# Optimization experiments

Measured on AMD Instinct MI355X. Metric: run time of the kernel, lower is better.

The kernel has to match this reference:

```python
import jax, jax.numpy as jnp
import numpy as np
import math

N_LAYER = 3
D = 256
NH = 4
MULT = 128
N = MULT * D // NH  # 8192
VOCAB = 256
EPS = 1e-5
TWO_PI = 2.0 * math.pi


def _get_freqs(n, theta=2.0 ** 16):
    t = jnp.arange(0, n, dtype=jnp.float32)
    q = jnp.floor(t / 2.0) * 2.0  # quantize to pairs
    return 1.0 / (theta ** (q / n)) / TWO_PI  # [N]


def _ln(x):
    # LayerNorm over last dim, no affine
    mu = jnp.mean(x, axis=-1, keepdims=True)
    var = jnp.var(x, axis=-1, keepdims=True)
    return (x - mu) / jnp.sqrt(var + EPS)


def _rope(phases, v):
    # phases: [T, N] (cycles); v: [..., T, N]
    ph = (phases % 1.0) * TWO_PI
    c, s = jnp.cos(ph), jnp.sin(ph)
    v_rot = jnp.stack((-v[..., 1::2], v[..., ::2]), axis=-1).reshape(v.shape)
    return v * c + v_rot * s


def setup_inputs() -> dict:
    key = jax.random.key(0)
    ks = jax.random.split(key, 6)
    B, T = 1, 1024
    std = 0.02
    return {
        "idx": jax.random.randint(ks[0], (B, T), 0, VOCAB),
        "embed": jax.random.normal(ks[1], (VOCAB, D), jnp.float32) * std,
        "encoder": jax.random.normal(ks[2], (NH, D, N), jnp.float32) * std,
        "encoder_v": jax.random.normal(ks[3], (NH, D, N), jnp.float32) * std,
        "decoder": jax.random.normal(ks[4], (NH * N, D), jnp.float32) * std,
        "lm_head": jax.random.normal(ks[5], (D, VOCAB), jnp.float32) * std,
    }


def reference(idx, embed, encoder, encoder_v, decoder, lm_head):
    B, T = idx.shape
    freqs = _get_freqs(N)  # [N]
    phases = jnp.arange(T, dtype=jnp.float32)[:, None] * freqs[None, :]  # [T, N]
    # strict lower triangular causal mask (diagonal excluded)
    causal = jnp.tril(jnp.ones((T, T), dtype=jnp.bool_), k=-1)

    x = _ln(embed[idx])  # [B, T, D]
    for _ in range(N_LAYER):
        # encoder projection + ReLU sparsification: [B, nh, T, N]
        x_sparse = jax.nn.relu(jnp.einsum('btd,hdn->bhtn', x, encoder))
        # RoPE on Q (= K)
        qr = _rope(phases, x_sparse)
        # unnormalized bilinear causal attention (no softmax)
        scores = jnp.einsum('bhtn,bhsn->bhts', qr, qr)
        scores = jnp.where(causal, scores, 0.0)
        ykv = _ln(jnp.einsum('bhts,bsd->bhtd', scores, x))  # [B, nh, T, D]
        y_sparse = jax.nn.relu(jnp.einsum('bhtd,hdn->bhtn', ykv, encoder_v))
        xy = x_sparse * y_sparse  # [B, nh, T, N]
        # MLP decode: head-major flatten of (nh, N) matches decoder rows
        ymlp = jnp.einsum('bhtn,btd... wrong', xy) if False else (
            xy.transpose(0, 2, 1, 3).reshape(B, T, NH * N) @ decoder)  # [B, T, D]
        x = _ln(x + _ln(ymlp))
    logits = x @ lm_head  # [B, T, VOCAB]
    return logits
```

## Files before the change

kernel.cpp:

```cpp
#include <hip/hip_runtime.h>
#include <hip/hip_bf16.h>
#include <math.h>
#include <stdint.h>

#define T_SEQ 1024
#define D_DIM 256
#define NH_C 4
#define N_DIM 8192
#define VOCAB_C 256
#define NLAYER 3
#define TWO_PI_F 6.283185307179586f
#define KSPLIT_DEC 32
#define KSPLIT_SC 2

typedef __bf16 bf16x8 __attribute__((ext_vector_type(8)));
typedef float f32x4 __attribute__((ext_vector_type(4)));

__device__ __forceinline__ unsigned short f2bf(float f) {
  unsigned u = __builtin_bit_cast(unsigned, f);
  u += 0x7fffu + ((u >> 16) & 1u);
  return (unsigned short)(u >> 16);
}
__device__ __forceinline__ float bf2f(unsigned short h) {
  unsigned u = ((unsigned)h) << 16;
  return __builtin_bit_cast(float, u);
}
__device__ __forceinline__ unsigned pack2(float a, float b) {
  return (unsigned)f2bf(a) | ((unsigned)f2bf(b) << 16);
}

typedef __attribute__((address_space(3))) uint32_t lds_u32;
typedef __attribute__((address_space(1))) const uint32_t glob_u32;
__device__ __forceinline__ void gload_lds16(const void* g, void* l) {
  __builtin_amdgcn_global_load_lds(reinterpret_cast<glob_u32*>(reinterpret_cast<uintptr_t>(g)),
                                   reinterpret_cast<lds_u32*>(reinterpret_cast<uintptr_t>(l)), 16, 0,
                                   0);
}

__global__ void k_transpose(const float* __restrict__ src, unsigned short* __restrict__ dst,
                            int R, int C, long sB, long dB) {
  __shared__ float tile[32][33];
  const int b = blockIdx.z;
  src += (size_t)b * sB;
  dst += (size_t)b * dB;
  const int c0 = blockIdx.x * 32, r0 = blockIdx.y * 32;
  const int tx = threadIdx.x, ty = threadIdx.y;
#pragma unroll
  for (int i = 0; i < 32; i += 8)
    tile[ty + i][tx] = src[(size_t)(r0 + ty + i) * C + (c0 + tx)];
  __syncthreads();
#pragma unroll
  for (int i = 0; i < 32; i += 8)
    dst[(size_t)(c0 + ty + i) * R + (r0 + tx)] = f2bf(tile[tx][ty + i]);
}

__global__ void k_ropetab(unsigned* __restrict__ cs) {
  const int id = blockIdx.x * 256 + threadIdx.x;
  const int pair = id >> 10, t = id & 1023;
  const float freq = exp2f(-(float)pair * (1.0f / 256.0f)) * (1.0f / TWO_PI_F);
  float ph = (float)t * freq;
  ph -= floorf(ph);
  float s, c;
  __sincosf(ph * TWO_PI_F, &s, &c);
  cs[id] = pack2(c, s);
}

__device__ __forceinline__ void stats256(float4 v, float& mu, float& rs) {
  float s = v.x + v.y + v.z + v.w;
  float ss = v.x * v.x + v.y * v.y + v.z * v.z + v.w * v.w;
#pragma unroll
  for (int o = 1; o < 64; o <<= 1) { s += __shfl_xor(s, o); ss += __shfl_xor(ss, o); }
  mu = s * (1.0f / 256.0f);
  float var = ss * (1.0f / 256.0f) - mu * mu;
  rs = rsqrtf(var + 1e-5f);
}

__global__ void k_embed_ln(const int* __restrict__ idx, const float* __restrict__ embed,
                           float* __restrict__ x, unsigned short* __restrict__ xb,
                           unsigned short* __restrict__ xT) {
  const int t = blockIdx.x, lane = threadIdx.x;
  const float* row = embed + (size_t)idx[t] * D_DIM;
  float4 v = ((const float4*)row)[lane];
  float mu, rs;
  stats256(v, mu, rs);
  float4 o = make_float4((v.x - mu) * rs, (v.y - mu) * rs, (v.z - mu) * rs, (v.w - mu) * rs);
  ((float4*)(x + (size_t)t * D_DIM))[lane] = o;
  ((uint2*)(xb + (size_t)t * D_DIM))[lane] = make_uint2(pack2(o.x, o.y), pack2(o.z, o.w));
  const int d0 = lane * 4;
  xT[(size_t)(d0 + 0) * T_SEQ + t] = f2bf(o.x);
  xT[(size_t)(d0 + 1) * T_SEQ + t] = f2bf(o.y);
  xT[(size_t)(d0 + 2) * T_SEQ + t] = f2bf(o.z);
  xT[(size_t)(d0 + 3) * T_SEQ + t] = f2bf(o.w);
}

__global__ void k_ln_rows(const float* __restrict__ in, unsigned short* __restrict__ outb) {
  const int r = blockIdx.x, lane = threadIdx.x;
  float4 v = ((const float4*)(in + (size_t)r * D_DIM))[lane];
  float mu, rs;
  stats256(v, mu, rs);
  ((uint2*)(outb + (size_t)r * D_DIM))[lane] =
      make_uint2(pack2((v.x - mu) * rs, (v.y - mu) * rs), pack2((v.z - mu) * rs, (v.w - mu) * rs));
}

template <int NP>
__global__ void k_update_x(const float* __restrict__ ymlp, float* __restrict__ x,
                           unsigned short* __restrict__ xb, unsigned short* __restrict__ xT) {
  const int t = blockIdx.x, lane = threadIdx.x;
  float4 m = make_float4(0.f, 0.f, 0.f, 0.f);
#pragma unroll
  for (int pp = 0; pp < NP; ++pp) {
    float4 q = ((const float4*)(ymlp + (size_t)pp * T_SEQ * D_DIM + (size_t)t * D_DIM))[lane];
    m.x += q.x; m.y += q.y; m.z += q.z; m.w += q.w;
  }
  float mu1, rs1;
  stats256(m, mu1, rs1);
  float4 xv = ((const float4*)(x + (size_t)t * D_DIM))[lane];
  float4 z = make_float4(xv.x + (m.x - mu1) * rs1, xv.y + (m.y - mu1) * rs1,
                         xv.z + (m.z - mu1) * rs1, xv.w + (m.w - mu1) * rs1);
  float mu2, rs2;
  stats256(z, mu2, rs2);
  float4 o = make_float4((z.x - mu2) * rs2, (z.y - mu2) * rs2, (z.z - mu2) * rs2, (z.w - mu2) * rs2);
  ((float4*)(x + (size_t)t * D_DIM))[lane] = o;
  ((uint2*)(xb + (size_t)t * D_DIM))[lane] = make_uint2(pack2(o.x, o.y), pack2(o.z, o.w));
  const int d0 = lane * 4;
  xT[(size_t)(d0 + 0) * T_SEQ + t] = f2bf(o.x);
  xT[(size_t)(d0 + 1) * T_SEQ + t] = f2bf(o.y);
  xT[(size_t)(d0 + 2) * T_SEQ + t] = f2bf(o.z);
  xT[(size_t)(d0 + 3) * T_SEQ + t] = f2bf(o.w);
}

template <int NP>
__global__ void k_comb(const float* __restrict__ sp, unsigned short* __restrict__ sc) {
  const size_t gid = (size_t)blockIdx.x * 256 + threadIdx.x;
  const size_t e0 = gid * 8;
  const int s = (int)(e0 & (T_SEQ - 1));
  const int t = (int)((e0 >> 10) & (T_SEQ - 1));
  if (s >= t) return;
  const int h = (int)(e0 >> 20);
  float v[8] = {0.f, 0.f, 0.f, 0.f, 0.f, 0.f, 0.f, 0.f};
#pragma unroll
  for (int pp = 0; pp < NP; ++pp) {
    const float* a = sp + ((size_t)(h * NP + pp)) * T_SEQ * T_SEQ + (size_t)t * T_SEQ + s;
    float4 a0 = *(const float4*)a, a1 = *(const float4*)(a + 4);
    v[0] += a0.x; v[1] += a0.y; v[2] += a0.z; v[3] += a0.w;
    v[4] += a1.x; v[5] += a1.y; v[6] += a1.z; v[7] += a1.w;
  }
  unsigned short o[8];
#pragma unroll
  for (int j = 0; j < 8; ++j) o[j] = (s + j < t) ? f2bf(v[j]) : (unsigned short)0;
  *(uint4*)(sc + e0) = *(uint4*)o;
}

template <int MODE, int BM, int BN, bool TRI_A, bool SWAPXY>
__global__ __launch_bounds__(256) void k_gemm(const unsigned short* __restrict__ A, long lda, long sAz,
                                              const unsigned short* __restrict__ B, long ldb, long sBz,
                                              void* __restrict__ Cv, long ldc, long sCz,
                                              const unsigned short* __restrict__ extra, long sEz,
                                              unsigned short* __restrict__ C2,
                                              const unsigned* __restrict__ ctab, int Ksize) {
  constexpr int MF = BM / 32;
  constexpr int NF = BN / 32;
  constexpr int BUFB = (BM + BN) * 128;

  const unsigned nbx = gridDim.x, nby = gridDim.y;
  const unsigned total = nbx * nby * gridDim.z;
  const unsigned lid = (blockIdx.z * nby + blockIdx.y) * nbx + blockIdx.x;
  const unsigned qq = total >> 3, rr = total & 7;
  const unsigned xcd = lid & 7, loc = lid >> 3;
  const unsigned wg = (xcd < rr ? xcd * (qq + 1) : rr * (qq + 1) + (xcd - rr) * qq) + loc;

  int bx, by, bz, zAB, kbase = 0;
  if constexpr (MODE == 2 || MODE == 6) {
    constexpr int NRT = T_SEQ / BM;
    constexpr int TPH = NRT * (NRT + 1) / 2;
    const int zz = wg / TPH;
    const int tt = wg % TPH;
    by = (int)((sqrtf(8.0f * (float)tt + 1.0f) - 1.0f) * 0.5f);
    if (by > NRT - 1) by = NRT - 1;
    while ((by + 1) * (by + 2) / 2 <= tt) ++by;
    while (by * (by + 1) / 2 > tt) --by;
    bx = tt - by * (by + 1) / 2;
    bz = zz;
    if constexpr (MODE == 6) {
      zAB = zz >> 1;
      kbase = (zz & 1) * Ksize;
    } else {
      zAB = zz;
    }
  } else if constexpr (SWAPXY) {
    by = wg % nby;
    bx = (wg / nby) % nbx;
    bz = wg / (nbx * nby);
    zAB = bz;
  } else {
    bx = wg % nbx;
    by = (wg / nbx) % nby;
    bz = wg / (nbx * nby);
    zAB = bz;
  }
  if constexpr (MODE == 7) kbase = bz * Ksize;

  const int i0 = by * BM;
  const int j0 = bx * BN;

  A += (size_t)zAB * sAz;
  B += (size_t)zAB * sBz;
  float* Cf = (float*)Cv + (size_t)bz * sCz;
  unsigned short* Ch = (unsigned short*)Cv + (size_t)bz * sCz;
  unsigned short* C2h = C2 ? C2 + (size_t)bz * sCz : nullptr;
  const unsigned short* E = extra ? extra + (size_t)bz * sEz : nullptr;

  const int tid = threadIdx.x;
  const int lane = tid & 63, w = tid >> 6;
  const int wr = w >> 1, wc = w & 1;

  __shared__ __align__(16) char lds[2 * BUFB];

  f32x4 acc[MF][NF];
#pragma unroll
  for (int m = 0; m < MF; ++m)
#pragma unroll
    for (int n = 0; n < NF; ++n) acc[m][n] = f32x4{0.f, 0.f, 0.f, 0.f};

  const char* Abytes = (const char*)A;
  const char* Bbytes = (const char*)B;
  const size_t ldab = (size_t)((MODE == 7) ? N_DIM : lda) * 2;
  const size_t ldbb = (size_t)ldb * 2;
  const int lr = lane >> 3;
  const int scol = ((lane & 7) * 16) ^ (lr << 4);

  auto stage = [&](int buf, int kt) {
    const int kk = kbase + kt * 64;
    const char* Ag;
    if constexpr (MODE == 7) {
      Ag = Abytes +
           ((size_t)(kk >> 13) * ((size_t)T_SEQ * N_DIM) + (size_t)i0 * N_DIM + (kk & (N_DIM - 1))) * 2;
    } else {
      Ag = Abytes + ((size_t)i0 * lda + kk) * 2;
    }
    const char* Bg = Bbytes + ((size_t)j0 * ldb + kk) * 2;
    char* lb = lds + buf * BUFB;
#pragma unroll
    for (int it = 0; it < BM / 32; ++it) {
      const int r0 = (w + 4 * it) * 8;
      gload_lds16(Ag + (size_t)(r0 + lr) * ldab + scol, lb + r0 * 128);
    }
#pragma unroll
    for (int it = 0; it < BN / 32; ++it) {
      const int r0 = (w + 4 * it) * 8;
      gload_lds16(Bg + (size_t)(r0 + lr) * ldbb + scol, lb + BM * 128 + r0 * 128);
    }
  };

  const int ar = lane & 15;
  const int ko16 = (lane >> 4) * 16;
  const int swz = (lane & 7) << 4;

  auto compute = [&](const char* Ab) {
    const char* Bb = Ab + BM * 128;
    bf16x8 af[2][MF], bfr[2][NF];
#pragma unroll
    for (int kk = 0; kk < 2; ++kk) {
      const int koff = (kk * 64 + ko16) ^ swz;
#pragma unroll
      for (int m = 0; m < MF; ++m)
        af[kk][m] = *(const bf16x8*)(Ab + (size_t)(wr * (BM / 2) + m * 16 + ar) * 128 + koff);
#pragma unroll
      for (int n = 0; n < NF; ++n)
        bfr[kk][n] = *(const bf16x8*)(Bb + (size_t)(wc * (BN / 2) + n * 16 + ar) * 128 + koff);
    }
#pragma unroll
    for (int kk = 0; kk < 2; ++kk)
#pragma unroll
      for (int m = 0; m < MF; ++m)
#pragma unroll
        for (int n = 0; n < NF; ++n)
          acc[m][n] = __builtin_amdgcn_mfma_f32_16x16x32_bf16(af[kk][m], bfr[kk][n], acc[m][n], 0, 0, 0);
  };

  const int nt = TRI_A ? (i0 / 64 + BM / 64) : Ksize / 64;
  stage(0, 0);
  __syncthreads();
  int cur = 0;
  for (int t = 0; t < nt; ++t) {
    if (t + 1 < nt) stage(cur ^ 1, t + 1);
    compute(lds + cur * BUFB);
    __syncthreads();
    cur ^= 1;
  }

#pragma unroll
  for (int m = 0; m < MF; ++m) {
    const int row0 = i0 + wr * (BM / 2) + m * 16 + ((lane >> 4) << 2);
#pragma unroll
    for (int n = 0; n < NF; ++n) {
      const int col = j0 + wc * (BN / 2) + n * 16 + (lane & 15);
      f32x4 c = acc[m][n];
      if constexpr (MODE == 4) {
        const uint4 q = *(const uint4*)(ctab + (size_t)(col >> 1) * T_SEQ + row0);
        const unsigned qw[4] = {q.x, q.y, q.z, q.w};
        const float sgn = (lane & 1) ? 1.f : -1.f;
#pragma unroll
        for (int r = 0; r < 4; ++r) {
          const float v = fmaxf(c[r], 0.f);
          const float pv = __shfl_xor(v, 1);
          const float cc = bf2f((unsigned short)(qw[r] & 0xffffu));
          const float ss = bf2f((unsigned short)(qw[r] >> 16));
          Ch[(size_t)(row0 + r) * ldc + col] = f2bf(v);
          C2h[(size_t)(row0 + r) * ldc + col] = f2bf(v * cc + sgn * pv * ss);
        }
      } else {
#pragma unroll
        for (int r = 0; r < 4; ++r) {
          const int row = row0 + r;
          const float v = c[r];
          if constexpr (MODE == 0 || MODE == 6 || MODE == 7) {
            Cf[(size_t)row * ldc + col] = v;
          } else if constexpr (MODE == 2) {
            Ch[(size_t)row * ldc + col] = (col < row) ? f2bf(v) : (unsigned short)0;
          } else if constexpr (MODE == 3) {
            float g = bf2f(E[(size_t)row * ldc + col]);
            Ch[(size_t)row * ldc + col] = f2bf(fmaxf(v, 0.f) * g);
          }
        }
      }
    }
  }
}

extern "C" void kernel_launch(void* const* d_in, const int* in_sizes, int n_in,
                              void* d_out, int out_size, void* d_ws, size_t ws_size,
                              hipStream_t stream) {
  const int* idx = (const int*)d_in[0];
  const float* embed = (const float*)d_in[1];
  const float* enc = (const float*)d_in[2];
  const float* encv = (const float*)d_in[3];
  const float* dec = (const float*)d_in[4];
  const float* lmh = (const float*)d_in[5];
  float* out = (float*)d_out;

  char* p = (char*)d_ws;
  auto carve = [&](size_t bytes) -> void* {
    void* r = (void*)p;
    p += (bytes + 255) & ~(size_t)255;
    return r;
  };
  unsigned short* encT = (unsigned short*)carve((size_t)NH_C * N_DIM * D_DIM * 2);
  unsigned short* encvT = (unsigned short*)carve((size_t)NH_C * N_DIM * D_DIM * 2);
  unsigned short* decT = (unsigned short*)carve((size_t)D_DIM * NH_C * N_DIM * 2);
  unsigned short* lmT = (unsigned short*)carve((size_t)VOCAB_C * D_DIM * 2);
  float* x = (float*)carve((size_t)T_SEQ * D_DIM * 4);
  unsigned short* xb = (unsigned short*)carve((size_t)T_SEQ * D_DIM * 2);
  unsigned short* xT = (unsigned short*)carve((size_t)D_DIM * T_SEQ * 2);
  unsigned short* xs = (unsigned short*)carve((size_t)NH_C * T_SEQ * N_DIM * 2);
  unsigned short* qr = (unsigned short*)carve((size_t)NH_C * T_SEQ * N_DIM * 2);
  unsigned short* sc = (unsigned short*)carve((size_t)NH_C * T_SEQ * T_SEQ * 2);
  float* ykv = (float*)carve((size_t)NH_C * T_SEQ * D_DIM * 4);
  unsigned short* ykvln = (unsigned short*)carve((size_t)NH_C * T_SEQ * D_DIM * 2);
  float* ymlp = (float*)carve((size_t)KSPLIT_DEC * T_SEQ * D_DIM * 4);
  unsigned* cstab = (unsigned*)carve((size_t)(N_DIM / 2) * T_SEQ * 4);
  float* scf32 = (float*)carve((size_t)KSPLIT_SC * NH_C * T_SEQ * T_SEQ * 4);
  const bool split_ok = ((size_t)(p - (char*)d_ws) <= ws_size);

  const dim3 tb32(32, 8);
  k_transpose<<<dim3(N_DIM / 32, D_DIM / 32, NH_C), tb32, 0, stream>>>(
      enc, encT, D_DIM, N_DIM, (long)D_DIM * N_DIM, (long)N_DIM * D_DIM);
  k_transpose<<<dim3(N_DIM / 32, D_DIM / 32, NH_C), tb32, 0, stream>>>(
      encv, encvT, D_DIM, N_DIM, (long)D_DIM * N_DIM, (long)N_DIM * D_DIM);
  k_transpose<<<dim3(D_DIM / 32, (NH_C * N_DIM) / 32, 1), tb32, 0, stream>>>(
      dec, decT, NH_C * N_DIM, D_DIM, 0, 0);
  k_transpose<<<dim3(VOCAB_C / 32, D_DIM / 32, 1), tb32, 0, stream>>>(lmh, lmT, D_DIM, VOCAB_C, 0, 0);
  k_ropetab<<<((N_DIM / 2) * T_SEQ) / 256, 256, 0, stream>>>(cstab);
  k_embed_ln<<<T_SEQ, 64, 0, stream>>>(idx, embed, x, xb, xT);
  (void)hipMemsetAsync(sc, 0, (size_t)NH_C * T_SEQ * T_SEQ * 2, stream);

  for (int l = 0; l < NLAYER; ++l) {
    k_gemm<4, 128, 128, false, true><<<dim3(N_DIM / 128, T_SEQ / 128, NH_C), 256, 0, stream>>>(
        xb, D_DIM, 0, encT, D_DIM, (long)N_DIM * D_DIM, xs, N_DIM, (long)T_SEQ * N_DIM, nullptr, 0,
        qr, cstab, D_DIM);
    if (split_ok) {
      k_gemm<6, 128, 128, false, false>
          <<<dim3(KSPLIT_SC * NH_C * (T_SEQ / 128) * (T_SEQ / 128 + 1) / 2, 1, 1), 256, 0, stream>>>(
              qr, N_DIM, (long)T_SEQ * N_DIM, qr, N_DIM, (long)T_SEQ * N_DIM, scf32, T_SEQ,
              (long)T_SEQ * T_SEQ, nullptr, 0, nullptr, nullptr, N_DIM / KSPLIT_SC);
      k_comb<KSPLIT_SC><<<(NH_C * T_SEQ * T_SEQ / 8) / 256, 256, 0, stream>>>(scf32, sc);
    } else {
      k_gemm<2, 64, 64, false, false>
          <<<dim3(NH_C * (T_SEQ / 64) * (T_SEQ / 64 + 1) / 2, 1, 1), 256, 0, stream>>>(
              qr, N_DIM, (long)T_SEQ * N_DIM, qr, N_DIM, (long)T_SEQ * N_DIM, sc, T_SEQ,
              (long)T_SEQ * T_SEQ, nullptr, 0, nullptr, nullptr, N_DIM);
    }
    k_gemm<0, 64, 64, true, false><<<dim3(D_DIM / 64, T_SEQ / 64, NH_C), 256, 0, stream>>>(
        sc, T_SEQ, (long)T_SEQ * T_SEQ, xT, T_SEQ, 0, ykv, D_DIM, (long)T_SEQ * D_DIM, nullptr, 0,
        nullptr, nullptr, T_SEQ);
    k_ln_rows<<<NH_C * T_SEQ, 64, 0, stream>>>(ykv, ykvln);
    k_gemm<3, 128, 128, false, true><<<dim3(N_DIM / 128, T_SEQ / 128, NH_C), 256, 0, stream>>>(
        ykvln, D_DIM, (long)T_SEQ * D_DIM, encvT, D_DIM, (long)N_DIM * D_DIM, qr, N_DIM,
        (long)T_SEQ * N_DIM, xs, (long)T_SEQ * N_DIM, nullptr, nullptr, D_DIM);
    k_gemm<7, 128, 128, false, false>
        <<<dim3(D_DIM / 128, T_SEQ / 128, KSPLIT_DEC), 256, 0, stream>>>(
            qr, N_DIM, 0, decT, (long)(NH_C * N_DIM), 0, ymlp, D_DIM, (long)T_SEQ * D_DIM,
            nullptr, 0, nullptr, nullptr, (NH_C * N_DIM) / KSPLIT_DEC);
    k_update_x<KSPLIT_DEC><<<T_SEQ, 64, 0, stream>>>(ymlp, x, xb, xT);
  }
  k_gemm<0, 64, 64, false, false><<<dim3(VOCAB_C / 64, T_SEQ / 64, 1), 256, 0, stream>>>(
      xb, D_DIM, 0, lmT, D_DIM, 0, out, VOCAB_C, 0, nullptr, 0, nullptr, nullptr, D_DIM);
}
```

Before: 667.1 us.

## Drop x_sparse buffer by inverting RoPE from qr in gate epilogue

The encoder GEMM now writes only the rotated qr tensor, stored as packed pairs, instead of both x_sparse and qr. The encoder_v GEMM recovers x_sparse by applying the inverse rotation to qr in place and uses it as the gate. This removes one large bf16 write and read per layer and frees workspace, which lets the score split-K be raised from 2 to 4. The trade-off is extra bf16 rounding on the recovered gate and in-place aliasing of qr.

```diff
diff --git a/kernel.cpp b/kernel.cpp
--- a/kernel.cpp
+++ b/kernel.cpp
@@ -11,7 +11,7 @@
 #define NLAYER 3
 #define TWO_PI_F 6.283185307179586f
 #define KSPLIT_DEC 32
-#define KSPLIT_SC 2
+#define KSPLIT_SC 4
 
 typedef __bf16 bf16x8 __attribute__((ext_vector_type(8)));
 typedef float f32x4 __attribute__((ext_vector_type(4)));
@@ -154,8 +154,8 @@
 template <int MODE, int BM, int BN, bool TRI_A, bool SWAPXY>
 __global__ __launch_bounds__(256) void k_gemm(const unsigned short* __restrict__ A, long lda, long sAz,
                                               const unsigned short* __restrict__ B, long ldb, long sBz,
-                                              void* __restrict__ Cv, long ldc, long sCz,
-                                              const unsigned short* __restrict__ extra, long sEz,
+                                              void* Cv, long ldc, long sCz,
+                                              const unsigned short* extra, long sEz,
                                               unsigned short* __restrict__ C2,
                                               const unsigned* __restrict__ ctab, int Ksize) {
   constexpr int MF = BM / 32;
@@ -182,8 +182,8 @@
     bx = tt - by * (by + 1) / 2;
     bz = zz;
     if constexpr (MODE == 6) {
-      zAB = zz >> 1;
-      kbase = (zz & 1) * Ksize;
+      zAB = zz / KSPLIT_SC;
+      kbase = (zz % KSPLIT_SC) * Ksize;
     } else {
       zAB = zz;
     }
@@ -207,7 +207,6 @@
   B += (size_t)zAB * sBz;
   float* Cf = (float*)Cv + (size_t)bz * sCz;
   unsigned short* Ch = (unsigned short*)Cv + (size_t)bz * sCz;
-  unsigned short* C2h = C2 ? C2 + (size_t)bz * sCz : nullptr;
   const unsigned short* E = extra ? extra + (size_t)bz * sEz : nullptr;
 
   const int tid = threadIdx.x;
@@ -299,15 +298,32 @@
       if constexpr (MODE == 4) {
         const uint4 q = *(const uint4*)(ctab + (size_t)(col >> 1) * T_SEQ + row0);
         const unsigned qw[4] = {q.x, q.y, q.z, q.w};
-        const float sgn = (lane & 1) ? 1.f : -1.f;
+        unsigned wpk[4];
 #pragma unroll
         for (int r = 0; r < 4; ++r) {
           const float v = fmaxf(c[r], 0.f);
           const float pv = __shfl_xor(v, 1);
+          const float x0 = (lane & 1) ? pv : v;
+          const float x1 = (lane & 1) ? v : pv;
           const float cc = bf2f((unsigned short)(qw[r] & 0xffffu));
           const float ss = bf2f((unsigned short)(qw[r] >> 16));
-          Ch[(size_t)(row0 + r) * ldc + col] = f2bf(v);
-          C2h[(size_t)(row0 + r) * ldc + col] = f2bf(v * cc + sgn * pv * ss);
+          wpk[r] = pack2(x0 * cc - x1 * ss, x1 * cc + x0 * ss);
+        }
+        const int rb = (lane & 1) * 2;
+        ((unsigned*)(Ch + (size_t)(row0 + rb) * ldc))[col >> 1] = wpk[rb];
+        ((unsigned*)(Ch + (size_t)(row0 + rb + 1) * ldc))[col >> 1] = wpk[rb + 1];
+      } else if constexpr (MODE == 3) {
+        const uint4 q4 = *(const uint4*)(ctab + (size_t)(col >> 1) * T_SEQ + row0);
+        const unsigned qw[4] = {q4.x, q4.y, q4.z, q4.w};
+        const float sgn = (lane & 1) ? 1.f : -1.f;
+#pragma unroll
+        for (int r = 0; r < 4; ++r) {
+          const float qv = bf2f(E[(size_t)(row0 + r) * ldc + col]);
+          const float pq = __shfl_xor(qv, 1);
+          const float cc = bf2f((unsigned short)(qw[r] & 0xffffu));
+          const float ss = bf2f((unsigned short)(qw[r] >> 16));
+          const float gate = fmaxf(qv * cc - sgn * pq * ss, 0.f);
+          Ch[(size_t)(row0 + r) * ldc + col] = f2bf(fmaxf(c[r], 0.f) * gate);
         }
       } else {
 #pragma unroll
@@ -318,9 +334,6 @@
             Cf[(size_t)row * ldc + col] = v;
           } else if constexpr (MODE == 2) {
             Ch[(size_t)row * ldc + col] = (col < row) ? f2bf(v) : (unsigned short)0;
-          } else if constexpr (MODE == 3) {
-            float g = bf2f(E[(size_t)row * ldc + col]);
-            Ch[(size_t)row * ldc + col] = f2bf(fmaxf(v, 0.f) * g);
           }
         }
       }
@@ -352,14 +365,13 @@
   float* x = (float*)carve((size_t)T_SEQ * D_DIM * 4);
   unsigned short* xb = (unsigned short*)carve((size_t)T_SEQ * D_DIM * 2);
   unsigned short* xT = (unsigned short*)carve((size_t)D_DIM * T_SEQ * 2);
-  unsigned short* xs = (unsigned short*)carve((size_t)NH_C * T_SEQ * N_DIM * 2);
+  float* scf32 = (float*)carve((size_t)KSPLIT_SC * NH_C * T_SEQ * T_SEQ * 4);
   unsigned short* qr = (unsigned short*)carve((size_t)NH_C * T_SEQ * N_DIM * 2);
   unsigned short* sc = (unsigned short*)carve((size_t)NH_C * T_SEQ * T_SEQ * 2);
   float* ykv = (float*)carve((size_t)NH_C * T_SEQ * D_DIM * 4);
   unsigned short* ykvln = (unsigned short*)carve((size_t)NH_C * T_SEQ * D_DIM * 2);
   float* ymlp = (float*)carve((size_t)KSPLIT_DEC * T_SEQ * D_DIM * 4);
   unsigned* cstab = (unsigned*)carve((size_t)(N_DIM / 2) * T_SEQ * 4);
-  float* scf32 = (float*)carve((size_t)KSPLIT_SC * NH_C * T_SEQ * T_SEQ * 4);
   const bool split_ok = ((size_t)(p - (char*)d_ws) <= ws_size);
 
   const dim3 tb32(32, 8);
@@ -376,8 +388,8 @@
 
   for (int l = 0; l < NLAYER; ++l) {
     k_gemm<4, 128, 128, false, true><<<dim3(N_DIM / 128, T_SEQ / 128, NH_C), 256, 0, stream>>>(
-        xb, D_DIM, 0, encT, D_DIM, (long)N_DIM * D_DIM, xs, N_DIM, (long)T_SEQ * N_DIM, nullptr, 0,
-        qr, cstab, D_DIM);
+        xb, D_DIM, 0, encT, D_DIM, (long)N_DIM * D_DIM, qr, N_DIM, (long)T_SEQ * N_DIM, nullptr, 0,
+        nullptr, cstab, D_DIM);
     if (split_ok) {
       k_gemm<6, 128, 128, false, false>
           <<<dim3(KSPLIT_SC * NH_C * (T_SEQ / 128) * (T_SEQ / 128 + 1) / 2, 1, 1), 256, 0, stream>>>(
@@ -396,7 +408,7 @@
     k_ln_rows<<<NH_C * T_SEQ, 64, 0, stream>>>(ykv, ykvln);
     k_gemm<3, 128, 128, false, true><<<dim3(N_DIM / 128, T_SEQ / 128, NH_C), 256, 0, stream>>>(
         ykvln, D_DIM, (long)T_SEQ * D_DIM, encvT, D_DIM, (long)N_DIM * D_DIM, qr, N_DIM,
-        (long)T_SEQ * N_DIM, xs, (long)T_SEQ * N_DIM, nullptr, nullptr, D_DIM);
+        (long)T_SEQ * N_DIM, qr, (long)T_SEQ * N_DIM, nullptr, cstab, D_DIM);
     k_gemm<7, 128, 128, false, false>
         <<<dim3(D_DIM / 128, T_SEQ / 128, KSPLIT_DEC), 256, 0, stream>>>(
             qr, N_DIM, 0, decT, (long)(NH_C * N_DIM), 0, ymlp, D_DIM, (long)T_SEQ * D_DIM,
```

Result: slower. 778.4 us (+16.7%).
